# Performance work log

Measured on AMD Instinct MI355X. Metric: run time of the kernel, lower is better.

## Reference

```python
import jax, jax.numpy as jnp
import numpy as np

BS, N, C = 16, 128, 512
EPS = 1e-5


def setup_inputs() -> dict:
    key = jax.random.key(0)
    ks = jax.random.split(key, 6)
    x = jax.random.normal(ks[0], (BS, N, C), dtype=jnp.float32)
    y = jax.random.normal(ks[1], (BS, C), dtype=jnp.float32)
    # edge conv: Conv2d(2C -> 1, 1x1), init std sqrt(2/(1*1*1))
    conv_e_w = jax.random.normal(ks[2], (1, 2 * C), dtype=jnp.float32) * np.sqrt(2.0)
    conv_e_b = jnp.zeros((1,), dtype=jnp.float32)
    bn_e_g = jnp.ones((1,), dtype=jnp.float32)
    bn_e_b = jnp.zeros((1,), dtype=jnp.float32)
    bn_e_m = jnp.zeros((1,), dtype=jnp.float32)
    bn_e_v = jnp.ones((1,), dtype=jnp.float32)
    # feature conv: Conv2d(2C -> C, 1x1), init std sqrt(2/C)
    conv_f_w = jax.random.normal(ks[3], (C, 2 * C), dtype=jnp.float32) * np.sqrt(2.0 / C)
    conv_f_b = jnp.zeros((C,), dtype=jnp.float32)
    bn_f_g = jnp.ones((C,), dtype=jnp.float32)
    bn_f_b = jnp.zeros((C,), dtype=jnp.float32)
    bn_f_m = jnp.zeros((C,), dtype=jnp.float32)
    bn_f_v = jnp.ones((C,), dtype=jnp.float32)
    return {
        "x": x, "y": y,
        "conv_e_w": conv_e_w, "conv_e_b": conv_e_b,
        "bn_e_g": bn_e_g, "bn_e_b": bn_e_b, "bn_e_m": bn_e_m, "bn_e_v": bn_e_v,
        "conv_f_w": conv_f_w, "conv_f_b": conv_f_b,
        "bn_f_g": bn_f_g, "bn_f_b": bn_f_b, "bn_f_m": bn_f_m, "bn_f_v": bn_f_v,
    }


def reference(x, y, conv_e_w, conv_e_b, bn_e_g, bn_e_b, bn_e_m, bn_e_v,
              conv_f_w, conv_f_b, bn_f_g, bn_f_b, bn_f_m, bn_f_v):
    bs, n, c = x.shape
    # ---- Wcompute: pairwise |x_i - x_j| -> conv1x1(2C->1) + BN + mask + softmax ----
    diff = jnp.abs(x[:, :, None, :] - x[:, None, :, :])  # [bs, N, N, C]
    w_diff = conv_e_w[0, :c]   # weights on pairwise-diff channels
    w_y = conv_e_w[0, c:]      # weights on broadcast y channels
    # 1x1 conv collapses to einsum; y part is constant over (i, j)
    score = (jnp.einsum('bijc,c->bij', diff, w_diff)
             + (y @ w_y)[:, None, None] + conv_e_b[0])  # [bs, N, N]
    # BatchNorm2d(1), inference mode
    score = (score - bn_e_m[0]) * (bn_e_g[0] * jax.lax.rsqrt(bn_e_v[0] + EPS)) + bn_e_b[0]
    # mask diagonal (W_id * 1e8) then softmax over neighbors j
    score = score - jnp.eye(n, dtype=score.dtype)[None] * 1e8
    W = jax.nn.softmax(score, axis=2)  # [bs, N, N]
    # ---- Gconv: neighbor aggregation + conv1x1(2C->C) + BN + ReLU ----
    x_nb = jnp.einsum('bij,bjc->bic', W, x)       # [bs, N, C]
    h = jnp.concatenate([x, x_nb], axis=2)        # [bs, N, 2C]
    out = jnp.einsum('bnk,ck->bnc', h, conv_f_w) + conv_f_b  # [bs, N, C]
    # BatchNorm2d(C), inference mode (per-channel)
    out = (out - bn_f_m) * (bn_f_g * jax.lax.rsqrt(bn_f_v + EPS)) + bn_f_b
    return jax.nn.relu(out)
```

## Files before the change

### kernel.cpp

```cpp
#include <hip/hip_runtime.h>
#include <hip/hip_bf16.h>

#define NTOK 128
#define CHN  512
#define KTOT 1024
#define EPSV 1e-5f
#define XNB_LD 520

typedef __attribute__((ext_vector_type(8))) short bf16x8;
typedef __attribute__((ext_vector_type(4))) float f32x4;

union BfPack4 { ushort4 u; __hip_bfloat16 h[4]; };


__global__ __launch_bounds__(256)
void k1a_scores(const float* __restrict__ xg,
                const float* __restrict__ wde,
                float* __restrict__ part)
{
    __shared__ float xs[64 * 129];
    const int bk = blockIdx.x;
    const int s  = bk & 7;
    const int ib = (bk >> 3) & 15;
    const int b  = bk >> 7;
    const int i0 = ib * 8;
    const int c0 = s * 64;
    const int t  = threadIdx.x;
    const float* __restrict__ xb = xg + (size_t)b * NTOK * CHN;

    const int cq = t & 15, jb = t >> 4;
    #pragma unroll
    for (int u = 0; u < 8; ++u) {
        const int j = jb + 16 * u;
        float4 v = *(const float4*)&xb[(size_t)j * CHN + c0 + cq * 4];
        xs[(cq * 4 + 0) * 129 + j] = v.x;
        xs[(cq * 4 + 1) * 129 + j] = v.y;
        xs[(cq * 4 + 2) * 129 + j] = v.z;
        xs[(cq * 4 + 3) * 129 + j] = v.w;
    }
    __syncthreads();

    const int j  = t & 127;
    const int rh = t >> 7;
    const float* xip = xb + (size_t)(i0 + rh * 4) * CHN + c0;

    float acc[4] = {0.f, 0.f, 0.f, 0.f};
    #pragma unroll 4
    for (int g = 0; g < 16; ++g) {
        const float4 wd  = *(const float4*)&wde[c0 + g * 4];
        const float4 xi0 = *(const float4*)&xip[0 * CHN + g * 4];
        const float4 xi1 = *(const float4*)&xip[1 * CHN + g * 4];
        const float4 xi2 = *(const float4*)&xip[2 * CHN + g * 4];
        const float4 xi3 = *(const float4*)&xip[3 * CHN + g * 4];
        const float xj0 = xs[(g * 4 + 0) * 129 + j];
        const float xj1 = xs[(g * 4 + 1) * 129 + j];
        const float xj2 = xs[(g * 4 + 2) * 129 + j];
        const float xj3 = xs[(g * 4 + 3) * 129 + j];
        acc[0] += fabsf(xi0.x - xj0) * wd.x + fabsf(xi0.y - xj1) * wd.y
                + fabsf(xi0.z - xj2) * wd.z + fabsf(xi0.w - xj3) * wd.w;
        acc[1] += fabsf(xi1.x - xj0) * wd.x + fabsf(xi1.y - xj1) * wd.y
                + fabsf(xi1.z - xj2) * wd.z + fabsf(xi1.w - xj3) * wd.w;
        acc[2] += fabsf(xi2.x - xj0) * wd.x + fabsf(xi2.y - xj1) * wd.y
                + fabsf(xi2.z - xj2) * wd.z + fabsf(xi2.w - xj3) * wd.w;
        acc[3] += fabsf(xi3.x - xj0) * wd.x + fabsf(xi3.y - xj1) * wd.y
                + fabsf(xi3.z - xj2) * wd.z + fabsf(xi3.w - xj3) * wd.w;
    }

    float* pp = part + ((size_t)s * 16 + b) * (NTOK * NTOK)
              + (size_t)(i0 + rh * 4) * NTOK + j;
    pp[0 * NTOK] = acc[0];
    pp[1 * NTOK] = acc[1];
    pp[2 * NTOK] = acc[2];
    pp[3 * NTOK] = acc[3];
}

__global__ __launch_bounds__(256)
void k0_prep(const float* __restrict__ xg,
             const float* __restrict__ wf,
             __hip_bfloat16* __restrict__ xbf,
             __hip_bfloat16* __restrict__ xTbf,
             __hip_bfloat16* __restrict__ wfb)
{
    __shared__ float ts[64 * 68];
    const int t  = threadIdx.x;
    const int bk = blockIdx.x;
    const int b  = bk >> 4;
    const int jt = (bk >> 3) & 1;
    const int ct = bk & 7;
    const int j0 = jt * 64, c0 = ct * 64;

    {
        const float* wr = wf + (size_t)(2 * bk) * KTOT;
        __hip_bfloat16* wo = wfb + (size_t)(2 * bk) * KTOT;
        #pragma unroll
        for (int u = 0; u < 2; ++u) {
            const int idx = t + u * 256;
            float4 v = *(const float4*)&wr[idx * 4];
            BfPack4 p;
            p.h[0]=__float2bfloat16(v.x); p.h[1]=__float2bfloat16(v.y);
            p.h[2]=__float2bfloat16(v.z); p.h[3]=__float2bfloat16(v.w);
            *(ushort4*)&wo[idx * 4] = p.u;
        }
    }

    const int jr = t >> 2, qd = t & 3;
    const float* src = xg + ((size_t)(b * NTOK) + j0 + jr) * CHN + c0 + qd * 16;
    float4 v0 = *(const float4*)&src[0];
    float4 v1 = *(const float4*)&src[4];
    float4 v2 = *(const float4*)&src[8];
    float4 v3 = *(const float4*)&src[12];
    *(float4*)&ts[jr * 68 + qd * 16 + 0]  = v0;
    *(float4*)&ts[jr * 68 + qd * 16 + 4]  = v1;
    *(float4*)&ts[jr * 68 + qd * 16 + 8]  = v2;
    *(float4*)&ts[jr * 68 + qd * 16 + 12] = v3;

    {
        __hip_bfloat16* hrow = xbf + ((size_t)(b * NTOK) + j0 + jr) * CHN + c0 + qd * 16;
        BfPack4 p;
        p.h[0]=__float2bfloat16(v0.x); p.h[1]=__float2bfloat16(v0.y);
        p.h[2]=__float2bfloat16(v0.z); p.h[3]=__float2bfloat16(v0.w);
        *(ushort4*)&hrow[0] = p.u;
        p.h[0]=__float2bfloat16(v1.x); p.h[1]=__float2bfloat16(v1.y);
        p.h[2]=__float2bfloat16(v1.z); p.h[3]=__float2bfloat16(v1.w);
        *(ushort4*)&hrow[4] = p.u;
        p.h[0]=__float2bfloat16(v2.x); p.h[1]=__float2bfloat16(v2.y);
        p.h[2]=__float2bfloat16(v2.z); p.h[3]=__float2bfloat16(v2.w);
        *(ushort4*)&hrow[8] = p.u;
        p.h[0]=__float2bfloat16(v3.x); p.h[1]=__float2bfloat16(v3.y);
        p.h[2]=__float2bfloat16(v3.z); p.h[3]=__float2bfloat16(v3.w);
        *(ushort4*)&hrow[12] = p.u;
    }
    __syncthreads();

    const int cs = t >> 4, jj = (t & 15) * 4;
    #pragma unroll
    for (int m = 0; m < 4; ++m) {
        const int c = cs + 16 * m;
        BfPack4 p;
        p.h[0] = __float2bfloat16(ts[(jj + 0) * 68 + c]);
        p.h[1] = __float2bfloat16(ts[(jj + 1) * 68 + c]);
        p.h[2] = __float2bfloat16(ts[(jj + 2) * 68 + c]);
        p.h[3] = __float2bfloat16(ts[(jj + 3) * 68 + c]);
        *(ushort4*)&xTbf[((size_t)(b * CHN) + c0 + c) * NTOK + j0 + jj] = p.u;
    }
}

__global__ __launch_bounds__(128)
void k1b_softmax(const float* __restrict__ part,
                 const float* __restrict__ bn_e_g,
                 const float* __restrict__ bn_e_v,
                 __hip_bfloat16* __restrict__ Wbf)
{
    const int bk = blockIdx.x;
    const int b  = bk >> 6;
    const int i  = (bk & 63) * 2 + (threadIdx.x >> 6);
    const int l  = threadIdx.x & 63;

    const float* pp = part + (size_t)(b * NTOK + i) * NTOK;
    float p1 = 0.f, p2 = 0.f;
    #pragma unroll
    for (int s = 0; s < 8; ++s) {
        p1 += pp[(size_t)s * 16 * NTOK * NTOK + l];
        p2 += pp[(size_t)s * 16 * NTOK * NTOK + l + 64];
    }
    const float sc = bn_e_g[0] * rsqrtf(bn_e_v[0] + EPSV);
    float l1 = p1 * sc - (l == i ? 1e8f : 0.f);
    float l2 = p2 * sc - (l + 64 == i ? 1e8f : 0.f);

    float m = fmaxf(l1, l2);
    #pragma unroll
    for (int off = 32; off > 0; off >>= 1) m = fmaxf(m, __shfl_xor(m, off));
    const float e1 = __expf(l1 - m);
    const float e2 = __expf(l2 - m);
    float ssum = e1 + e2;
    #pragma unroll
    for (int off = 32; off > 0; off >>= 1) ssum += __shfl_xor(ssum, off);
    const float inv = 1.f / ssum;

    __hip_bfloat16* wr = Wbf + (size_t)(b * NTOK + i) * NTOK;
    wr[l]      = __float2bfloat16(e1 * inv);
    wr[l + 64] = __float2bfloat16(e2 * inv);
}

__global__ __launch_bounds__(256)
void k2_fused(const __hip_bfloat16* __restrict__ Wbf,
              const __hip_bfloat16* __restrict__ xTbf,
              const __hip_bfloat16* __restrict__ xbf,
              const __hip_bfloat16* __restrict__ wfb,
              const float* __restrict__ fb,
              const float* __restrict__ gg,
              const float* __restrict__ bb,
              const float* __restrict__ mm,
              const float* __restrict__ vv,
              float* __restrict__ out)
{
    __shared__ unsigned short xnb[64 * XNB_LD];
    const int blk = blockIdx.x;
    const int rt  = blk >> 3;
    const int ct  = blk & 7;
    const int b   = rt >> 1;
    const int i0  = (rt & 1) * 64;
    const int c0  = ct * 64;
    const int t    = threadIdx.x;
    const int w    = t >> 6;
    const int lane = t & 63;
    const int m16  = lane & 15;
    const int q    = lane >> 4;

    {
        const int n0w = w * 128;
        #pragma unroll
        for (int mt = 0; mt < 4; ++mt) {
            const short* Ar = (const short*)Wbf
                            + (size_t)(b * NTOK + i0 + mt * 16 + m16) * NTOK + q * 8;
            const bf16x8 a0 = *(const bf16x8*)(Ar + 0);
            const bf16x8 a1 = *(const bf16x8*)(Ar + 32);
            const bf16x8 a2 = *(const bf16x8*)(Ar + 64);
            const bf16x8 a3 = *(const bf16x8*)(Ar + 96);
            #pragma unroll
            for (int nt = 0; nt < 8; ++nt) {
                const int n = n0w + nt * 16;
                const short* Br = (const short*)xTbf
                                + ((size_t)(b * CHN) + n + m16) * NTOK + q * 8;
                f32x4 acc = {0.f, 0.f, 0.f, 0.f};
                acc = __builtin_amdgcn_mfma_f32_16x16x32_bf16(a0, *(const bf16x8*)(Br + 0),  acc, 0, 0, 0);
                acc = __builtin_amdgcn_mfma_f32_16x16x32_bf16(a1, *(const bf16x8*)(Br + 32), acc, 0, 0, 0);
                acc = __builtin_amdgcn_mfma_f32_16x16x32_bf16(a2, *(const bf16x8*)(Br + 64), acc, 0, 0, 0);
                acc = __builtin_amdgcn_mfma_f32_16x16x32_bf16(a3, *(const bf16x8*)(Br + 96), acc, 0, 0, 0);
                #pragma unroll
                for (int r = 0; r < 4; ++r) {
                    __hip_bfloat16 hv = __float2bfloat16(acc[r]);
                    xnb[(mt * 16 + q * 4 + r) * XNB_LD + n + m16] =
                        *(unsigned short*)&hv;
                }
            }
        }
    }
    __syncthreads();

    const int wm = w & 1;
    const int wn = w >> 1;

    const short* AL = (const short*)xbf
                    + (size_t)(b * NTOK + i0 + wm * 32 + m16) * CHN + q * 8;
    const short* BW = (const short*)wfb
                    + (size_t)(c0 + wn * 32 + m16) * KTOT + q * 8;
    const unsigned short* AR = &xnb[(wm * 32 + m16) * XNB_LD + q * 8];

    f32x4 acc00 = {0.f, 0.f, 0.f, 0.f};
    f32x4 acc01 = acc00, acc10 = acc00, acc11 = acc00;

    #pragma unroll 4
    for (int k0 = 0; k0 < 512; k0 += 32) {
        const bf16x8 aA = *(const bf16x8*)(AL + k0);
        const bf16x8 aB = *(const bf16x8*)(AL + 16 * CHN + k0);
        const bf16x8 bA = *(const bf16x8*)(BW + k0);
        const bf16x8 bB = *(const bf16x8*)(BW + 16 * KTOT + k0);
        acc00 = __builtin_amdgcn_mfma_f32_16x16x32_bf16(aA, bA, acc00, 0, 0, 0);
        acc01 = __builtin_amdgcn_mfma_f32_16x16x32_bf16(aA, bB, acc01, 0, 0, 0);
        acc10 = __builtin_amdgcn_mfma_f32_16x16x32_bf16(aB, bA, acc10, 0, 0, 0);
        acc11 = __builtin_amdgcn_mfma_f32_16x16x32_bf16(aB, bB, acc11, 0, 0, 0);
    }
    #pragma unroll 4
    for (int k0 = 0; k0 < 512; k0 += 32) {
        const bf16x8 aA = *(const bf16x8*)(AR + k0);
        const bf16x8 aB = *(const bf16x8*)(AR + 16 * XNB_LD + k0);
        const bf16x8 bA = *(const bf16x8*)(BW + 512 + k0);
        const bf16x8 bB = *(const bf16x8*)(BW + 16 * KTOT + 512 + k0);
        acc00 = __builtin_amdgcn_mfma_f32_16x16x32_bf16(aA, bA, acc00, 0, 0, 0);
        acc01 = __builtin_amdgcn_mfma_f32_16x16x32_bf16(aA, bB, acc01, 0, 0, 0);
        acc10 = __builtin_amdgcn_mfma_f32_16x16x32_bf16(aB, bA, acc10, 0, 0, 0);
        acc11 = __builtin_amdgcn_mfma_f32_16x16x32_bf16(aB, bB, acc11, 0, 0, 0);
    }

    #pragma unroll
    for (int ni = 0; ni < 2; ++ni) {
        const int c = c0 + wn * 32 + ni * 16 + m16;
        const float gf = gg[c] * rsqrtf(vv[c] + EPSV);
        const float ad = fb[c] - mm[c];
        const float bv = bb[c];
        const f32x4 acr0 = ni ? acc01 : acc00;
        const f32x4 acr1 = ni ? acc11 : acc10;
        #pragma unroll
        for (int r2 = 0; r2 < 4; ++r2) {
            int row = b * NTOK + i0 + wm * 32 + q * 4 + r2;
            float val = (acr0[r2] + ad) * gf + bv;
            out[(size_t)row * CHN + c] = fmaxf(val, 0.f);
            row += 16;
            val = (acr1[r2] + ad) * gf + bv;
            out[(size_t)row * CHN + c] = fmaxf(val, 0.f);
        }
    }
}

extern "C" void kernel_launch(void* const* d_in, const int* in_sizes, int n_in,
                              void* d_out, int out_size, void* d_ws, size_t ws_size,
                              hipStream_t stream) {
    const float* x        = (const float*)d_in[0];
    const float* conv_e_w = (const float*)d_in[2];
    const float* bn_e_g   = (const float*)d_in[4];
    const float* bn_e_v   = (const float*)d_in[7];
    const float* conv_f_w = (const float*)d_in[8];
    const float* conv_f_b = (const float*)d_in[9];
    const float* bn_f_g   = (const float*)d_in[10];
    const float* bn_f_b   = (const float*)d_in[11];
    const float* bn_f_m   = (const float*)d_in[12];
    const float* bn_f_v   = (const float*)d_in[13];
    float* out = (float*)d_out;

    char* ws = (char*)d_ws;
    float*          part = (float*)(ws);
    __hip_bfloat16* Wbf  = (__hip_bfloat16*)(ws + (8u << 20));
    __hip_bfloat16* xTbf = (__hip_bfloat16*)(ws + (8u << 20) + (512u << 10));
    __hip_bfloat16* xbf  = (__hip_bfloat16*)(ws + (10u << 20) + (512u << 10));
    __hip_bfloat16* wfb  = (__hip_bfloat16*)(ws + (12u << 20) + (512u << 10));

    k1a_scores<<<2048, 256, 0, stream>>>(x, conv_e_w, part);
    k0_prep<<<256, 256, 0, stream>>>(x, conv_f_w, xbf, xTbf, wfb);
    k1b_softmax<<<1024, 128, 0, stream>>>(part, bn_e_g, bn_e_v, Wbf);
    k2_fused<<<256, 256, 0, stream>>>(Wbf, xTbf, xbf, wfb, conv_f_b,
                                      bn_f_g, bn_f_b, bn_f_m, bn_f_v, out);
}
```

Baseline: 139.7 us.

## Merge score and prep kernels; split aggregation GEMM into separate kernel

Folds the prep work into the score kernel as extra blocks, removing one launch. The old fused aggregation+GEMM kernel, which recomputed x_nb per column tile in shared memory, is split in two: one kernel writes x_nb into the right half of a concatenated bf16 h buffer, and another runs a single K=1024 GEMM with BN and ReLU. This removes the eightfold redundant W@x recomputation, at the cost of an extra launch and a global round trip for x_nb.

```diff
diff --git a/kernel.cpp b/kernel.cpp
--- a/kernel.cpp
+++ b/kernel.cpp
@@ -5,7 +5,6 @@
 #define CHN  512
 #define KTOT 1024
 #define EPSV 1e-5f
-#define XNB_LD 520
 
 typedef __attribute__((ext_vector_type(8))) short bf16x8;
 typedef __attribute__((ext_vector_type(4))) float f32x4;
@@ -14,142 +13,140 @@
 
 
 __global__ __launch_bounds__(256)
-void k1a_scores(const float* __restrict__ xg,
-                const float* __restrict__ wde,
-                float* __restrict__ part)
+void ka_scores_prep(const float* __restrict__ xg,
+                    const float* __restrict__ wde,
+                    const float* __restrict__ wf,
+                    float* __restrict__ part,
+                    __hip_bfloat16* __restrict__ hb,
+                    __hip_bfloat16* __restrict__ xTbf,
+                    __hip_bfloat16* __restrict__ wfb)
 {
     __shared__ float xs[64 * 129];
-    const int bk = blockIdx.x;
-    const int s  = bk & 7;
-    const int ib = (bk >> 3) & 15;
-    const int b  = bk >> 7;
-    const int i0 = ib * 8;
-    const int c0 = s * 64;
-    const int t  = threadIdx.x;
-    const float* __restrict__ xb = xg + (size_t)b * NTOK * CHN;
-
-    const int cq = t & 15, jb = t >> 4;
-    #pragma unroll
-    for (int u = 0; u < 8; ++u) {
-        const int j = jb + 16 * u;
-        float4 v = *(const float4*)&xb[(size_t)j * CHN + c0 + cq * 4];
-        xs[(cq * 4 + 0) * 129 + j] = v.x;
-        xs[(cq * 4 + 1) * 129 + j] = v.y;
-        xs[(cq * 4 + 2) * 129 + j] = v.z;
-        xs[(cq * 4 + 3) * 129 + j] = v.w;
-    }
-    __syncthreads();
-
-    const int j  = t & 127;
-    const int rh = t >> 7;
-    const float* xip = xb + (size_t)(i0 + rh * 4) * CHN + c0;
-
-    float acc[4] = {0.f, 0.f, 0.f, 0.f};
-    #pragma unroll 4
-    for (int g = 0; g < 16; ++g) {
-        const float4 wd  = *(const float4*)&wde[c0 + g * 4];
-        const float4 xi0 = *(const float4*)&xip[0 * CHN + g * 4];
-        const float4 xi1 = *(const float4*)&xip[1 * CHN + g * 4];
-        const float4 xi2 = *(const float4*)&xip[2 * CHN + g * 4];
-        const float4 xi3 = *(const float4*)&xip[3 * CHN + g * 4];
-        const float xj0 = xs[(g * 4 + 0) * 129 + j];
-        const float xj1 = xs[(g * 4 + 1) * 129 + j];
-        const float xj2 = xs[(g * 4 + 2) * 129 + j];
-        const float xj3 = xs[(g * 4 + 3) * 129 + j];
-        acc[0] += fabsf(xi0.x - xj0) * wd.x + fabsf(xi0.y - xj1) * wd.y
-                + fabsf(xi0.z - xj2) * wd.z + fabsf(xi0.w - xj3) * wd.w;
-        acc[1] += fabsf(xi1.x - xj0) * wd.x + fabsf(xi1.y - xj1) * wd.y
-                + fabsf(xi1.z - xj2) * wd.z + fabsf(xi1.w - xj3) * wd.w;
-        acc[2] += fabsf(xi2.x - xj0) * wd.x + fabsf(xi2.y - xj1) * wd.y
-                + fabsf(xi2.z - xj2) * wd.z + fabsf(xi2.w - xj3) * wd.w;
-        acc[3] += fabsf(xi3.x - xj0) * wd.x + fabsf(xi3.y - xj1) * wd.y
-                + fabsf(xi3.z - xj2) * wd.z + fabsf(xi3.w - xj3) * wd.w;
-    }
-
-    float* pp = part + ((size_t)s * 16 + b) * (NTOK * NTOK)
-              + (size_t)(i0 + rh * 4) * NTOK + j;
-    pp[0 * NTOK] = acc[0];
-    pp[1 * NTOK] = acc[1];
-    pp[2 * NTOK] = acc[2];
-    pp[3 * NTOK] = acc[3];
-}
-
-__global__ __launch_bounds__(256)
-void k0_prep(const float* __restrict__ xg,
-             const float* __restrict__ wf,
-             __hip_bfloat16* __restrict__ xbf,
-             __hip_bfloat16* __restrict__ xTbf,
-             __hip_bfloat16* __restrict__ wfb)
-{
-    __shared__ float ts[64 * 68];
-    const int t  = threadIdx.x;
-    const int bk = blockIdx.x;
-    const int b  = bk >> 4;
-    const int jt = (bk >> 3) & 1;
-    const int ct = bk & 7;
-    const int j0 = jt * 64, c0 = ct * 64;
-
-    {
-        const float* wr = wf + (size_t)(2 * bk) * KTOT;
-        __hip_bfloat16* wo = wfb + (size_t)(2 * bk) * KTOT;
+    const int t = threadIdx.x;
+
+    if (blockIdx.x < 2048) {
+        const int bk = blockIdx.x;
+        const int s  = bk & 7;
+        const int ib = (bk >> 3) & 15;
+        const int b  = bk >> 7;
+        const int i0 = ib * 8;
+        const int c0 = s * 64;
+        const float* __restrict__ xb = xg + (size_t)b * NTOK * CHN;
+
+        const int cq = t & 15, jb = t >> 4;
         #pragma unroll
-        for (int u = 0; u < 2; ++u) {
-            const int idx = t + u * 256;
-            float4 v = *(const float4*)&wr[idx * 4];
+        for (int u = 0; u < 8; ++u) {
+            const int j = jb + 16 * u;
+            float4 v = *(const float4*)&xb[(size_t)j * CHN + c0 + cq * 4];
+            xs[(cq * 4 + 0) * 129 + j] = v.x;
+            xs[(cq * 4 + 1) * 129 + j] = v.y;
+            xs[(cq * 4 + 2) * 129 + j] = v.z;
+            xs[(cq * 4 + 3) * 129 + j] = v.w;
+        }
+        __syncthreads();
+
+        const int j  = t & 127;
+        const int rh = t >> 7;
+        const float* xip = xb + (size_t)(i0 + rh * 4) * CHN + c0;
+
+        float acc[4] = {0.f, 0.f, 0.f, 0.f};
+        #pragma unroll 4
+        for (int g = 0; g < 16; ++g) {
+            const float4 wd  = *(const float4*)&wde[c0 + g * 4];
+            const float4 xi0 = *(const float4*)&xip[0 * CHN + g * 4];
+            const float4 xi1 = *(const float4*)&xip[1 * CHN + g * 4];
+            const float4 xi2 = *(const float4*)&xip[2 * CHN + g * 4];
+            const float4 xi3 = *(const float4*)&xip[3 * CHN + g * 4];
+            const float xj0 = xs[(g * 4 + 0) * 129 + j];
+            const float xj1 = xs[(g * 4 + 1) * 129 + j];
+            const float xj2 = xs[(g * 4 + 2) * 129 + j];
+            const float xj3 = xs[(g * 4 + 3) * 129 + j];
+            acc[0] += fabsf(xi0.x - xj0) * wd.x + fabsf(xi0.y - xj1) * wd.y
+                    + fabsf(xi0.z - xj2) * wd.z + fabsf(xi0.w - xj3) * wd.w;
+            acc[1] += fabsf(xi1.x - xj0) * wd.x + fabsf(xi1.y - xj1) * wd.y
+                    + fabsf(xi1.z - xj2) * wd.z + fabsf(xi1.w - xj3) * wd.w;
+            acc[2] += fabsf(xi2.x - xj0) * wd.x + fabsf(xi2.y - xj1) * wd.y
+                    + fabsf(xi2.z - xj2) * wd.z + fabsf(xi2.w - xj3) * wd.w;
+            acc[3] += fabsf(xi3.x - xj0) * wd.x + fabsf(xi3.y - xj1) * wd.y
+                    + fabsf(xi3.z - xj2) * wd.z + fabsf(xi3.w - xj3) * wd.w;
+        }
+
+        float* pp = part + ((size_t)s * 16 + b) * (NTOK * NTOK)
+                  + (size_t)(i0 + rh * 4) * NTOK + j;
+        pp[0 * NTOK] = acc[0];
+        pp[1 * NTOK] = acc[1];
+        pp[2 * NTOK] = acc[2];
+        pp[3 * NTOK] = acc[3];
+    } else {
+        float* ts = xs;
+        const int bk = blockIdx.x - 2048;
+        const int b  = bk >> 4;
+        const int jt = (bk >> 3) & 1;
+        const int ct = bk & 7;
+        const int j0 = jt * 64, c0 = ct * 64;
+
+        {
+            const float* wr = wf + (size_t)(2 * bk) * KTOT;
+            __hip_bfloat16* wo = wfb + (size_t)(2 * bk) * KTOT;
+            #pragma unroll
+            for (int u = 0; u < 2; ++u) {
+                const int idx = t + u * 256;
+                float4 v = *(const float4*)&wr[idx * 4];
+                BfPack4 p;
+                p.h[0]=__float2bfloat16(v.x); p.h[1]=__float2bfloat16(v.y);
+                p.h[2]=__float2bfloat16(v.z); p.h[3]=__float2bfloat16(v.w);
+                *(ushort4*)&wo[idx * 4] = p.u;
+            }
+        }
+
+        const int jr = t >> 2, qd = t & 3;
+        const float* src = xg + ((size_t)(b * NTOK) + j0 + jr) * CHN + c0 + qd * 16;
+        float4 v0 = *(const float4*)&src[0];
+        float4 v1 = *(const float4*)&src[4];
+        float4 v2 = *(const float4*)&src[8];
+        float4 v3 = *(const float4*)&src[12];
+        *(float4*)&ts[jr * 68 + qd * 16 + 0]  = v0;
+        *(float4*)&ts[jr * 68 + qd * 16 + 4]  = v1;
+        *(float4*)&ts[jr * 68 + qd * 16 + 8]  = v2;
+        *(float4*)&ts[jr * 68 + qd * 16 + 12] = v3;
+
+        {
+            __hip_bfloat16* hrow = hb + ((size_t)(b * NTOK) + j0 + jr) * KTOT + c0 + qd * 16;
             BfPack4 p;
-            p.h[0]=__float2bfloat16(v.x); p.h[1]=__float2bfloat16(v.y);
-            p.h[2]=__float2bfloat16(v.z); p.h[3]=__float2bfloat16(v.w);
-            *(ushort4*)&wo[idx * 4] = p.u;
-        }
-    }
-
-    const int jr = t >> 2, qd = t & 3;
-    const float* src = xg + ((size_t)(b * NTOK) + j0 + jr) * CHN + c0 + qd * 16;
-    float4 v0 = *(const float4*)&src[0];
-    float4 v1 = *(const float4*)&src[4];
-    float4 v2 = *(const float4*)&src[8];
-    float4 v3 = *(const float4*)&src[12];
-    *(float4*)&ts[jr * 68 + qd * 16 + 0]  = v0;
-    *(float4*)&ts[jr * 68 + qd * 16 + 4]  = v1;
-    *(float4*)&ts[jr * 68 + qd * 16 + 8]  = v2;
-    *(float4*)&ts[jr * 68 + qd * 16 + 12] = v3;
-
-    {
-        __hip_bfloat16* hrow = xbf + ((size_t)(b * NTOK) + j0 + jr) * CHN + c0 + qd * 16;
-        BfPack4 p;
-        p.h[0]=__float2bfloat16(v0.x); p.h[1]=__float2bfloat16(v0.y);
-        p.h[2]=__float2bfloat16(v0.z); p.h[3]=__float2bfloat16(v0.w);
-        *(ushort4*)&hrow[0] = p.u;
-        p.h[0]=__float2bfloat16(v1.x); p.h[1]=__float2bfloat16(v1.y);
-        p.h[2]=__float2bfloat16(v1.z); p.h[3]=__float2bfloat16(v1.w);
-        *(ushort4*)&hrow[4] = p.u;
-        p.h[0]=__float2bfloat16(v2.x); p.h[1]=__float2bfloat16(v2.y);
-        p.h[2]=__float2bfloat16(v2.z); p.h[3]=__float2bfloat16(v2.w);
-        *(ushort4*)&hrow[8] = p.u;
-        p.h[0]=__float2bfloat16(v3.x); p.h[1]=__float2bfloat16(v3.y);
-        p.h[2]=__float2bfloat16(v3.z); p.h[3]=__float2bfloat16(v3.w);
-        *(ushort4*)&hrow[12] = p.u;
-    }
-    __syncthreads();
-
-    const int cs = t >> 4, jj = (t & 15) * 4;
-    #pragma unroll
-    for (int m = 0; m < 4; ++m) {
-        const int c = cs + 16 * m;
-        BfPack4 p;
-        p.h[0] = __float2bfloat16(ts[(jj + 0) * 68 + c]);
-        p.h[1] = __float2bfloat16(ts[(jj + 1) * 68 + c]);
-        p.h[2] = __float2bfloat16(ts[(jj + 2) * 68 + c]);
-        p.h[3] = __float2bfloat16(ts[(jj + 3) * 68 + c]);
-        *(ushort4*)&xTbf[((size_t)(b * CHN) + c0 + c) * NTOK + j0 + jj] = p.u;
+            p.h[0]=__float2bfloat16(v0.x); p.h[1]=__float2bfloat16(v0.y);
+            p.h[2]=__float2bfloat16(v0.z); p.h[3]=__float2bfloat16(v0.w);
+            *(ushort4*)&hrow[0] = p.u;
+            p.h[0]=__float2bfloat16(v1.x); p.h[1]=__float2bfloat16(v1.y);
+            p.h[2]=__float2bfloat16(v1.z); p.h[3]=__float2bfloat16(v1.w);
+            *(ushort4*)&hrow[4] = p.u;
+            p.h[0]=__float2bfloat16(v2.x); p.h[1]=__float2bfloat16(v2.y);
+            p.h[2]=__float2bfloat16(v2.z); p.h[3]=__float2bfloat16(v2.w);
+            *(ushort4*)&hrow[8] = p.u;
+            p.h[0]=__float2bfloat16(v3.x); p.h[1]=__float2bfloat16(v3.y);
+            p.h[2]=__float2bfloat16(v3.z); p.h[3]=__float2bfloat16(v3.w);
+            *(ushort4*)&hrow[12] = p.u;
+        }
+        __syncthreads();
+
+        const int cs = t >> 4, jj = (t & 15) * 4;
+        #pragma unroll
+        for (int m = 0; m < 4; ++m) {
+            const int c = cs + 16 * m;
+            BfPack4 p;
+            p.h[0] = __float2bfloat16(ts[(jj + 0) * 68 + c]);
+            p.h[1] = __float2bfloat16(ts[(jj + 1) * 68 + c]);
+            p.h[2] = __float2bfloat16(ts[(jj + 2) * 68 + c]);
+            p.h[3] = __float2bfloat16(ts[(jj + 3) * 68 + c]);
+            *(ushort4*)&xTbf[((size_t)(b * CHN) + c0 + c) * NTOK + j0 + jj] = p.u;
+        }
     }
 }
 
 __global__ __launch_bounds__(128)
-void k1b_softmax(const float* __restrict__ part,
-                 const float* __restrict__ bn_e_g,
-                 const float* __restrict__ bn_e_v,
-                 __hip_bfloat16* __restrict__ Wbf)
+void kb_softmax(const float* __restrict__ part,
+                const float* __restrict__ bn_e_g,
+                const float* __restrict__ bn_e_v,
+                __hip_bfloat16* __restrict__ Wbf)
 {
     const int bk = blockIdx.x;
     const int b  = bk >> 6;
@@ -183,90 +180,84 @@
 }
 
 __global__ __launch_bounds__(256)
-void k2_fused(const __hip_bfloat16* __restrict__ Wbf,
-              const __hip_bfloat16* __restrict__ xTbf,
-              const __hip_bfloat16* __restrict__ xbf,
-              const __hip_bfloat16* __restrict__ wfb,
-              const float* __restrict__ fb,
-              const float* __restrict__ gg,
-              const float* __restrict__ bb,
-              const float* __restrict__ mm,
-              const float* __restrict__ vv,
-              float* __restrict__ out)
+void kc_xnb(const __hip_bfloat16* __restrict__ Wbf,
+            const __hip_bfloat16* __restrict__ xTbf,
+            __hip_bfloat16* __restrict__ hb)
 {
-    __shared__ unsigned short xnb[64 * XNB_LD];
-    const int blk = blockIdx.x;
-    const int rt  = blk >> 3;
-    const int ct  = blk & 7;
-    const int b   = rt >> 1;
-    const int i0  = (rt & 1) * 64;
-    const int c0  = ct * 64;
+    const int bk = blockIdx.x;
+    const int t  = threadIdx.x;
+    const int b  = bk >> 5;
+    const int mt = (bk >> 3) & 3;
+    const int ct = bk & 7;
+    const int i0 = mt * 32, c0 = ct * 64;
+
+    const int w    = t >> 6;
+    const int lane = t & 63;
+    const int wm   = w & 1;
+    const int wn   = w >> 1;
+    const int m16  = lane & 15;
+    const int q    = lane >> 4;
+
+    const short* A0 = (const short*)Wbf  + (size_t)(b * NTOK + i0 + wm * 16 + m16) * NTOK + q * 8;
+    const short* B0 = (const short*)xTbf + ((size_t)(b * CHN) + c0 + wn * 32 + m16) * NTOK + q * 8;
+
+    f32x4 acc0 = {0.f, 0.f, 0.f, 0.f};
+    f32x4 acc1 = acc0;
+
+    #pragma unroll
+    for (int k0 = 0; k0 < NTOK; k0 += 32) {
+        const bf16x8 a  = *(const bf16x8*)(A0 + k0);
+        const bf16x8 b0 = *(const bf16x8*)(B0 + k0);
+        const bf16x8 b1 = *(const bf16x8*)(B0 + 16 * NTOK + k0);
+        acc0 = __builtin_amdgcn_mfma_f32_16x16x32_bf16(a, b0, acc0, 0, 0, 0);
+        acc1 = __builtin_amdgcn_mfma_f32_16x16x32_bf16(a, b1, acc1, 0, 0, 0);
+    }
+
+    #pragma unroll
+    for (int ni = 0; ni < 2; ++ni) {
+        const int c = c0 + wn * 32 + ni * 16 + m16;
+        const f32x4 ac = ni ? acc1 : acc0;
+        #pragma unroll
+        for (int r = 0; r < 4; ++r) {
+            const int i = i0 + wm * 16 + q * 4 + r;
+            hb[(size_t)(b * NTOK + i) * KTOT + CHN + c] = __float2bfloat16(ac[r]);
+        }
+    }
+}
+
+__global__ __launch_bounds__(256)
+void kd_gemm_bn_relu(const __hip_bfloat16* __restrict__ hbp,
+                     const __hip_bfloat16* __restrict__ wfbp,
+                     const float* __restrict__ fb,
+                     const float* __restrict__ gg,
+                     const float* __restrict__ bb,
+                     const float* __restrict__ mm,
+                     const float* __restrict__ vv,
+                     float* __restrict__ out)
+{
+    const int blk  = blockIdx.x;
+    const int r0   = (blk >> 3) << 6;
+    const int c0   = (blk & 7) << 6;
     const int t    = threadIdx.x;
     const int w    = t >> 6;
     const int lane = t & 63;
+    const int wm   = w & 1;
+    const int wn   = w >> 1;
     const int m16  = lane & 15;
-    const int q    = lane >> 4;
-
-    {
-        const int n0w = w * 128;
-        #pragma unroll
-        for (int mt = 0; mt < 4; ++mt) {
-            const short* Ar = (const short*)Wbf
-                            + (size_t)(b * NTOK + i0 + mt * 16 + m16) * NTOK + q * 8;
-            const bf16x8 a0 = *(const bf16x8*)(Ar + 0);
-            const bf16x8 a1 = *(const bf16x8*)(Ar + 32);
-            const bf16x8 a2 = *(const bf16x8*)(Ar + 64);
-            const bf16x8 a3 = *(const bf16x8*)(Ar + 96);
-            #pragma unroll
-            for (int nt = 0; nt < 8; ++nt) {
-                const int n = n0w + nt * 16;
-                const short* Br = (const short*)xTbf
-                                + ((size_t)(b * CHN) + n + m16) * NTOK + q * 8;
-                f32x4 acc = {0.f, 0.f, 0.f, 0.f};
-                acc = __builtin_amdgcn_mfma_f32_16x16x32_bf16(a0, *(const bf16x8*)(Br + 0),  acc, 0, 0, 0);
-                acc = __builtin_amdgcn_mfma_f32_16x16x32_bf16(a1, *(const bf16x8*)(Br + 32), acc, 0, 0, 0);
-                acc = __builtin_amdgcn_mfma_f32_16x16x32_bf16(a2, *(const bf16x8*)(Br + 64), acc, 0, 0, 0);
-                acc = __builtin_amdgcn_mfma_f32_16x16x32_bf16(a3, *(const bf16x8*)(Br + 96), acc, 0, 0, 0);
-                #pragma unroll
-                for (int r = 0; r < 4; ++r) {
-                    __hip_bfloat16 hv = __float2bfloat16(acc[r]);
-                    xnb[(mt * 16 + q * 4 + r) * XNB_LD + n + m16] =
-                        *(unsigned short*)&hv;
-                }
-            }
-        }
-    }
-    __syncthreads();
-
-    const int wm = w & 1;
-    const int wn = w >> 1;
-
-    const short* AL = (const short*)xbf
-                    + (size_t)(b * NTOK + i0 + wm * 32 + m16) * CHN + q * 8;
-    const short* BW = (const short*)wfb
-                    + (size_t)(c0 + wn * 32 + m16) * KTOT + q * 8;
-    const unsigned short* AR = &xnb[(wm * 32 + m16) * XNB_LD + q * 8];
+    const int qq   = lane >> 4;
+
+    const short* A0 = (const short*)hbp  + (size_t)(r0 + wm * 32 + m16) * KTOT + qq * 8;
+    const short* B0 = (const short*)wfbp + (size_t)(c0 + wn * 32 + m16) * KTOT + qq * 8;
 
     f32x4 acc00 = {0.f, 0.f, 0.f, 0.f};
     f32x4 acc01 = acc00, acc10 = acc00, acc11 = acc00;
 
     #pragma unroll 4
-    for (int k0 = 0; k0 < 512; k0 += 32) {
-        const bf16x8 aA = *(const bf16x8*)(AL + k0);
-        const bf16x8 aB = *(const bf16x8*)(AL + 16 * CHN + k0);
-        const bf16x8 bA = *(const bf16x8*)(BW + k0);
-        const bf16x8 bB = *(const bf16x8*)(BW + 16 * KTOT + k0);
-        acc00 = __builtin_amdgcn_mfma_f32_16x16x32_bf16(aA, bA, acc00, 0, 0, 0);
-        acc01 = __builtin_amdgcn_mfma_f32_16x16x32_bf16(aA, bB, acc01, 0, 0, 0);
-        acc10 = __builtin_amdgcn_mfma_f32_16x16x32_bf16(aB, bA, acc10, 0, 0, 0);
-        acc11 = __builtin_amdgcn_mfma_f32_16x16x32_bf16(aB, bB, acc11, 0, 0, 0);
-    }
-    #pragma unroll 4
-    for (int k0 = 0; k0 < 512; k0 += 32) {
-        const bf16x8 aA = *(const bf16x8*)(AR + k0);
-        const bf16x8 aB = *(const bf16x8*)(AR + 16 * XNB_LD + k0);
-        const bf16x8 bA = *(const bf16x8*)(BW + 512 + k0);
-        const bf16x8 bB = *(const bf16x8*)(BW + 16 * KTOT + 512 + k0);
+    for (int k0 = 0; k0 < KTOT; k0 += 32) {
+        const bf16x8 aA = *(const bf16x8*)(A0 + k0);
+        const bf16x8 aB = *(const bf16x8*)(A0 + 16 * KTOT + k0);
+        const bf16x8 bA = *(const bf16x8*)(B0 + k0);
+        const bf16x8 bB = *(const bf16x8*)(B0 + 16 * KTOT + k0);
         acc00 = __builtin_amdgcn_mfma_f32_16x16x32_bf16(aA, bA, acc00, 0, 0, 0);
         acc01 = __builtin_amdgcn_mfma_f32_16x16x32_bf16(aA, bB, acc01, 0, 0, 0);
         acc10 = __builtin_amdgcn_mfma_f32_16x16x32_bf16(aB, bA, acc10, 0, 0, 0);
@@ -283,7 +274,7 @@
         const f32x4 acr1 = ni ? acc11 : acc10;
         #pragma unroll
         for (int r2 = 0; r2 < 4; ++r2) {
-            int row = b * NTOK + i0 + wm * 32 + q * 4 + r2;
+            int row = r0 + wm * 32 + qq * 4 + r2;
             float val = (acr0[r2] + ad) * gf + bv;
             out[(size_t)row * CHN + c] = fmaxf(val, 0.f);
             row += 16;
@@ -310,14 +301,15 @@
 
     char* ws = (char*)d_ws;
     float*          part = (float*)(ws);
-    __hip_bfloat16* Wbf  = (__hip_bfloat16*)(ws + (8u << 20));
-    __hip_bfloat16* xTbf = (__hip_bfloat16*)(ws + (8u << 20) + (512u << 10));
-    __hip_bfloat16* xbf  = (__hip_bfloat16*)(ws + (10u << 20) + (512u << 10));
-    __hip_bfloat16* wfb  = (__hip_bfloat16*)(ws + (12u << 20) + (512u << 10));
-
-    k1a_scores<<<2048, 256, 0, stream>>>(x, conv_e_w, part);
-    k0_prep<<<256, 256, 0, stream>>>(x, conv_f_w, xbf, xTbf, wfb);
-    k1b_softmax<<<1024, 128, 0, stream>>>(part, bn_e_g, bn_e_v, Wbf);
-    k2_fused<<<256, 256, 0, stream>>>(Wbf, xTbf, xbf, wfb, conv_f_b,
-                                      bn_f_g, bn_f_b, bn_f_m, bn_f_v, out);
-}
+    __hip_bfloat16* hb   = (__hip_bfloat16*)(ws + (8u  << 20));
+    __hip_bfloat16* wfb  = (__hip_bfloat16*)(ws + (12u << 20));
+    __hip_bfloat16* Wbf  = (__hip_bfloat16*)(ws + (13u << 20));
+    __hip_bfloat16* xTbf = (__hip_bfloat16*)(ws + (13u << 20) + (512u << 10));
+
+    ka_scores_prep<<<2304, 256, 0, stream>>>(x, conv_e_w, conv_f_w,
+                                             part, hb, xTbf, wfb);
+    kb_softmax<<<1024, 128, 0, stream>>>(part, bn_e_g, bn_e_v, Wbf);
+    kc_xnb<<<512, 256, 0, stream>>>(Wbf, xTbf, hb);
+    kd_gemm_bn_relu<<<256, 256, 0, stream>>>(hb, wfb, conv_f_b, bn_f_g, bn_f_b,
+                                             bn_f_m, bn_f_v, out);
+}
```

Result: faster. 129.8 us (-7.1%).
